# Kernel optimization log

Hardware: AMD Instinct MI355X
Metric: run time of the kernel (lower is better)

The kernel has to match this reference:

```python
import jax, jax.numpy as jnp
import numpy as np

B, S, E, H, DH, F = 4, 2048, 1024, 4, 256, 4096


def setup_inputs() -> dict:
    key = jax.random.key(0)
    ks = jax.random.split(key, 16)
    def w(k, shape):
        return jax.random.normal(k, shape, jnp.float32) * 0.02
    return {
        "inputs": jax.random.normal(ks[0], (B, S, E), jnp.float32),
        "context": jax.random.normal(ks[1], (B, S, E), jnp.float32),
        # self-attention (causal) per-head projections stacked over heads
        "Wk1": w(ks[2], (H, E, DH)), "bk1": jnp.zeros((H, DH), jnp.float32),
        "Wq1": w(ks[3], (H, E, DH)), "bq1": jnp.zeros((H, DH), jnp.float32),
        "Wv1": w(ks[4], (H, E, DH)), "bv1": jnp.zeros((H, DH), jnp.float32),
        "Wo1": w(ks[5], (E, E)), "bo1": jnp.zeros((E,), jnp.float32),
        # cross-attention (no mask)
        "Wk2": w(ks[6], (H, E, DH)), "bk2": jnp.zeros((H, DH), jnp.float32),
        "Wq2": w(ks[7], (H, E, DH)), "bq2": jnp.zeros((H, DH), jnp.float32),
        "Wv2": w(ks[8], (H, E, DH)), "bv2": jnp.zeros((H, DH), jnp.float32),
        "Wo2": w(ks[9], (E, E)), "bo2": jnp.zeros((E,), jnp.float32),
        "ln_g": jnp.ones((E,), jnp.float32), "ln_b": jnp.zeros((E,), jnp.float32),
        # FFN
        "W1": w(ks[10], (E, F)), "b1": jnp.zeros((F,), jnp.float32),
        "W2": w(ks[11], (F, E)), "b2": jnp.zeros((E,), jnp.float32),
    }


def _mha(kin, vin, qin, Wk, bk, Wq, bq, Wv, bv, Wo, bo, causal):
    # per-head Dense projections, batched over heads: [B,S,E] x [H,E,DH] -> [B,H,S,DH]
    K = jnp.einsum('bse,hed->bhsd', kin, Wk) + bk[None, :, None, :]
    Q = jnp.einsum('bse,hed->bhsd', qin, Wq) + bq[None, :, None, :]
    V = jnp.einsum('bse,hed->bhsd', vin, Wv) + bv[None, :, None, :]
    # NOTE: original divides by head_dim (K.get_shape()[2]), NOT sqrt(head_dim)
    scores = jnp.einsum('bhqd,bhkd->bhqk', Q, K) / K.shape[-1]
    if causal:
        sq, sk = scores.shape[-2], scores.shape[-1]
        mask = jnp.triu(jnp.full((sq, sk), -jnp.inf, scores.dtype), k=1)
        scores = scores + mask  # additive -inf strictly above the diagonal
    A = jax.nn.softmax(scores, axis=-1)
    # concat heads in order along the feature axis, then output Dense
    out = jnp.einsum('bhqk,bhkd->bqhd', A, V).reshape(qin.shape[0], qin.shape[1], -1)
    return out @ Wo + bo


def _ln(x, g, b):
    # keras LayerNormalization default epsilon = 1e-3
    m = x.mean(-1, keepdims=True)
    v = ((x - m) ** 2).mean(-1, keepdims=True)
    return (x - m) / jnp.sqrt(v + 1e-3) * g + b


def reference(inputs, context, Wk1, bk1, Wq1, bq1, Wv1, bv1, Wo1, bo1,
              Wk2, bk2, Wq2, bq2, Wv2, bv2, Wo2, bo2,
              ln_g, ln_b, W1, b1, W2, b2):
    # dropout layers are identity at inference
    a = _mha(inputs, inputs, inputs, Wk1, bk1, Wq1, bq1, Wv1, bv1, Wo1, bo1, True) + inputs
    a = _ln(a, ln_g, ln_b)
    # cross-attention: keys/values = context, queries = normalized self-attn output
    c = _mha(context, context, a, Wk2, bk2, Wq2, bq2, Wv2, bv2, Wo2, bo2, False) + a
    c = _ln(c, ln_g, ln_b)
    h = jax.nn.relu(c @ W1 + b1) @ W2 + b2 + c
    return jax.nn.relu(_ln(h, ln_g, ln_b))
```

## Files before the change

kernel.cpp:

```cpp
#include <hip/hip_runtime.h>

#define DEV __device__ __forceinline__

typedef unsigned short u16;
typedef __bf16 bf16x8 __attribute__((ext_vector_type(8)));
typedef bf16x8 __attribute__((may_alias)) bf16x8a;
typedef float f32x4 __attribute__((ext_vector_type(4)));
typedef float f32x16 __attribute__((ext_vector_type(16)));

constexpr int NB = 4, NS = 2048, NE = 1024, NH = 4, NDH = 256, NF = 4096;
constexpr int NR = NB * NS;

DEV u16 f2bf(float f) {
  unsigned u = __float_as_uint(f);
  u += 0x7fff + ((u >> 16) & 1);
  return (u16)(u >> 16);
}

DEV f32x4 mfma16(bf16x8 a, bf16x8 b, f32x4 c) {
  return __builtin_amdgcn_mfma_f32_16x16x32_bf16(a, b, c, 0, 0, 0);
}
DEV f32x16 mfma32(bf16x8 a, bf16x8 b, f32x16 c) {
  return __builtin_amdgcn_mfma_f32_32x32x16_bf16(a, b, c, 0, 0, 0);
}

DEV bf16x8 ldfrag(const u16* p) { return *(const bf16x8a*)p; }

DEV void gload_lds16(const void* g, void* l) {
  __builtin_amdgcn_global_load_lds(
      (const __attribute__((address_space(1))) void*)g,
      (__attribute__((address_space(3))) void*)l, 16, 0, 0);
}

DEV void blockbar() {
  asm volatile("" ::: "memory");
  __builtin_amdgcn_s_barrier();
  asm volatile("" ::: "memory");
}

DEV unsigned packbf(float a, float b) {
  union { __bf16 h[2]; unsigned u; } x;
  x.h[0] = (__bf16)a; x.h[1] = (__bf16)b;
  return x.u;
}

__global__ void cast_f32_bf16(const float* __restrict__ in, u16* __restrict__ out, int n4) {
  int i = blockIdx.x * 256 + threadIdx.x;
  if (i >= n4) return;
  float4 v = ((const float4*)in)[i];
  ushort4 o;
  o.x = f2bf(v.x); o.y = f2bf(v.y); o.z = f2bf(v.z); o.w = f2bf(v.w);
  ((ushort4*)out)[i] = o;
}

__global__ void transpose_cast(const float* __restrict__ in, u16* __restrict__ out, int R, int C) {
  __shared__ float t[32][33];
  size_t base = (size_t)blockIdx.z * R * C;
  int c0 = blockIdx.x * 32, r0 = blockIdx.y * 32;
  int x = threadIdx.x;
  for (int yy = threadIdx.y; yy < 32; yy += 8)
    t[yy][x] = in[base + (size_t)(r0 + yy) * C + c0 + x];
  __syncthreads();
  for (int yy = threadIdx.y; yy < 32; yy += 8)
    out[base + (size_t)(c0 + yy) * R + r0 + x] = f2bf(t[x][yy]);
}

__global__ void transpose_cast6(const float* s0, const float* s1, const float* s2,
                                const float* s3, const float* s4, const float* s5,
                                u16* d0, u16* d1, u16* d2, u16* d3, u16* d4, u16* d5) {
  __shared__ float t[32][33];
  int z = blockIdx.z;
  int widx = z >> 2, hz = z & 3;
  const float* in; u16* out;
  switch (widx) {
    case 0: in = s0; out = d0; break;
    case 1: in = s1; out = d1; break;
    case 2: in = s2; out = d2; break;
    case 3: in = s3; out = d3; break;
    case 4: in = s4; out = d4; break;
    default: in = s5; out = d5; break;
  }
  size_t base = (size_t)hz * NE * NDH;
  int c0 = blockIdx.x * 32, r0 = blockIdx.y * 32;
  int x = threadIdx.x;
  for (int yy = threadIdx.y; yy < 32; yy += 8)
    t[yy][x] = in[base + (size_t)(r0 + yy) * NDH + c0 + x];
  __syncthreads();
  for (int yy = threadIdx.y; yy < 32; yy += 8)
    out[base + (size_t)(c0 + yy) * NE + r0 + x] = f2bf(t[x][yy]);
}

__global__ void transpose_cast2(const float* s0, const float* s1,
                                u16* d0, u16* d1) {
  __shared__ float t[32][33];
  const float* in = blockIdx.z ? s1 : s0;
  u16* out = blockIdx.z ? d1 : d0;
  int c0 = blockIdx.x * 32, r0 = blockIdx.y * 32;
  int x = threadIdx.x;
  for (int yy = threadIdx.y; yy < 32; yy += 8)
    t[yy][x] = in[(size_t)(r0 + yy) * NE + c0 + x];
  __syncthreads();
  for (int yy = threadIdx.y; yy < 32; yy += 8)
    out[(size_t)(c0 + yy) * NE + r0 + x] = f2bf(t[x][yy]);
}

__global__ void pack_bias(const float* b0, const float* b1, const float* b2,
                          const float* b3, const float* b4,
                          float* BQKV1, float* BKV2) {
  int x = blockIdx.x;
  int seg = x >> 2;
  int i = (x & 3) * 256 + threadIdx.x;
  switch (seg) {
    case 0: BQKV1[i] = b0[i]; break;
    case 1: BQKV1[1024 + i] = b1[i]; break;
    case 2: BQKV1[2048 + i] = b2[i]; break;
    case 3: BKV2[i] = b3[i]; break;
    default: BKV2[1024 + i] = b4[i]; break;
  }
}

__global__ void transpose_v(const u16* __restrict__ V, int vstride, u16* __restrict__ Vt) {
  __shared__ u16 t[32][34];
  int bh = blockIdx.z, b = bh >> 2, h = bh & (NH - 1);
  int s0 = blockIdx.x * 32, d0 = blockIdx.y * 32;
  int x = threadIdx.x;
  for (int yy = threadIdx.y; yy < 32; yy += 8)
    t[yy][x] = V[(size_t)(b * NS + s0 + yy) * vstride + h * NDH + d0 + x];
  __syncthreads();
  for (int yy = threadIdx.y; yy < 32; yy += 8)
    Vt[((size_t)bh * NDH + d0 + yy) * NS + s0 + x] = t[x][yy];
}

template<int OUTF32, int RELU>
__global__ __launch_bounds__(256, 2)
void gemm2b(const u16* __restrict__ A, const u16* __restrict__ Bt,
            const float* __restrict__ bias, const float* __restrict__ res,
            float* __restrict__ outF, u16* __restrict__ outB,
            int M, int N, int K)
{
  __shared__ __align__(16) u16 smem[32768];

  int tid = threadIdx.x, w = tid >> 6, lane = tid & 63;
  int lr = lane & 15, lk = lane >> 4;

  int flat = blockIdx.y * gridDim.x + blockIdx.x;
  int cpx = (gridDim.x * gridDim.y) >> 3;
  int swz = (flat & 7) * cpx + (flat >> 3);
  int bx = swz % gridDim.x, by = swz / gridDim.x;
  int rowBlk = by * 128, colBlk = bx * 128;

  f32x4 acc[8][2];
#pragma unroll
  for (int f = 0; f < 8; f++)
#pragma unroll
    for (int n = 0; n < 2; n++) acc[f][n] = (f32x4){0.f, 0.f, 0.f, 0.f};

  int srow = lane >> 3;
  int scol = ((lane & 7) ^ srow) * 8;

  const u16* gA = A + (size_t)rowBlk * K;
  const u16* gB = Bt + (size_t)colBlk * K;

  auto stageA = [&](int t, int p) {
#pragma unroll
    for (int j = 0; j < 4; j++) {
      int rbase = (w * 4 + j) * 8;
      gload_lds16(gA + (size_t)(rbase + srow) * K + (size_t)t * 64 + scol,
                  &smem[(p * 128 + rbase) * 64]);
    }
  };
  auto stageB = [&](int t, int p) {
#pragma unroll
    for (int j = 0; j < 4; j++) {
      int rbase = (w * 4 + j) * 8;
      gload_lds16(gB + (size_t)(rbase + srow) * K + (size_t)t * 64 + scol,
                  &smem[16384 + (p * 128 + rbase) * 64]);
    }
  };

  stageB(0, 0);
  asm volatile("" ::: "memory");
  stageA(0, 0);
  asm volatile("s_waitcnt vmcnt(0)" ::: "memory");
  blockbar();

  int NT = K >> 6;
  for (int t = 0; t < NT; t++) {
    int p = t & 1;
    if (t + 1 < NT) {
      stageB(t + 1, p ^ 1);
      asm volatile("" ::: "memory");
      stageA(t + 1, p ^ 1);
      asm volatile("" ::: "memory");
    }
    const u16* Ar = &smem[p * 8192];
    const u16* Br = &smem[16384 + p * 8192];
    bf16x8 bf[2][2], af[8][2];
#pragma unroll
    for (int n = 0; n < 2; n++)
#pragma unroll
      for (int s = 0; s < 2; s++) {
        int rowB = w * 32 + n * 16 + lr;
        bf[n][s] = ldfrag(&Br[rowB * 64 + (((s * 4 + lk) ^ (lr & 7)) * 8)]);
      }
#pragma unroll
    for (int f = 0; f < 8; f++)
#pragma unroll
      for (int s = 0; s < 2; s++) {
        int rowA = f * 16 + lr;
        af[f][s] = ldfrag(&Ar[rowA * 64 + (((s * 4 + lk) ^ (lr & 7)) * 8)]);
      }
    __builtin_amdgcn_s_setprio(1);
#pragma unroll
    for (int f = 0; f < 8; f++)
#pragma unroll
      for (int n = 0; n < 2; n++)
#pragma unroll
        for (int s = 0; s < 2; s++)
          acc[f][n] = mfma16(af[f][s], bf[n][s], acc[f][n]);
    __builtin_amdgcn_s_setprio(0);
    asm volatile("s_waitcnt vmcnt(0)" ::: "memory");
    blockbar();
  }

  int ocol0 = colBlk + w * 32;
#pragma unroll
  for (int n = 0; n < 2; n++) {
    int c = ocol0 + n * 16 + lr;
    float bv = bias[c];
#pragma unroll
    for (int f = 0; f < 8; f++) {
      int r0 = rowBlk + f * 16 + lk * 4;
#pragma unroll
      for (int j = 0; j < 4; j++) {
        float v = acc[f][n][j] + bv;
        if (OUTF32) v += res[(size_t)(r0 + j) * N + c];
        if (RELU) v = fmaxf(v, 0.f);
        if (OUTF32) outF[(size_t)(r0 + j) * N + c] = v;
        else        outB[(size_t)(r0 + j) * N + c] = f2bf(v);
      }
    }
  }
}

template<int CAUSAL, int SPLIT>
__global__ __launch_bounds__(512, 2)
void attn8w(const u16* __restrict__ Qp, int qstride,
            const u16* __restrict__ Kp, int kstride,
            const u16* __restrict__ Vt, u16* __restrict__ O,
            float* __restrict__ Op, float* __restrict__ ml)
{
  __shared__ __align__(16) u16 smem[65536];

  int bidx = blockIdx.x;
  int bh, qt, kt0, kt1;
  if (SPLIT) {
    int qtIdx = bidx >> 5;
    qt = 15 - qtIdx;
    int sub = bidx & 31;
    int half = sub >> 4;
    bh = sub & 15;
    kt0 = half ? (qt + 1) : 0;
    kt1 = half ? (2 * qt + 2) : (qt + 1);
  } else {
    bh = bidx & 15;
    qt = CAUSAL ? (15 - (bidx >> 4)) : (bidx >> 4);
    kt0 = 0;
    kt1 = CAUSAL ? (2 * qt + 2) : (NS / 64);
  }
  int b = bh >> 2, h = bh & 3;
  int tid = threadIdx.x, w = tid >> 6, lane = tid & 63;
  int L = lane & 31, hi = lane >> 5;
  int g = w >> 1, ks = w & 1;

  int qbase = qt * 128 + g * 32;

  const u16* qrow = Qp + (size_t)(b * NS + qbase + L) * qstride + h * NDH;
  bf16x8 qf[16];
#pragma unroll
  for (int s = 0; s < 16; s++) qf[s] = ldfrag(qrow + s * 16 + hi * 8);

  f32x16 oacc[8];
#pragma unroll
  for (int db = 0; db < 8; db++) oacc[db] = (f32x16){};
  float m = -1e30f, l = 0.f;

  constexpr float SC = 1.0f / NDH;

  const u16* kbase = Kp + (size_t)(b * NS) * kstride + h * NDH;
  const u16* vbase = Vt + (size_t)bh * NDH * NS;

  auto stage = [&](int kt, int buf) {
#pragma unroll
    for (int ii = 0; ii < 4; ii++) {
      int gi = w * 4 + ii;
      int krow = 2 * gi + hi;
      int kcol = L ^ (krow & 31);
      gload_lds16(kbase + (size_t)(kt * 64 + krow) * kstride + kcol * 8,
                  &smem[buf * 16384 + gi * 512]);
      int vd = gi * 8 + (lane >> 3);
      int vg = (lane & 7) ^ (vd & 7);
      gload_lds16(vbase + (size_t)vd * NS + kt * 64 + vg * 8,
                  &smem[32768 + buf * 16384 + gi * 512]);
    }
  };

  stage(kt0, 0);
  asm volatile("" ::: "memory");

  for (int kt = kt0; kt < kt1; kt++) {
    int buf = (kt - kt0) & 1;
    const u16* bK = &smem[buf * 16384];
    const u16* bV = &smem[32768 + buf * 16384];
    if (kt + 1 < kt1) {
      stage(kt + 1, buf ^ 1);
      asm volatile("s_waitcnt vmcnt(8)" ::: "memory");
    } else {
      asm volatile("s_waitcnt vmcnt(0)" ::: "memory");
    }
    blockbar();

    int ksub0 = kt * 64 + ks * 32;
    bool skip = CAUSAL && (ksub0 > qbase + 31);
    if (!skip) {
      bool domask = CAUSAL && (ksub0 + 31 > qbase);
      __builtin_amdgcn_s_setprio(1);
      f32x16 sa = (f32x16){};
#pragma unroll
      for (int s = 0; s < 16; s++) {
        int row = ks * 32 + L;
        bf16x8 kf = ldfrag(&bK[row * 256 + (((2 * s + hi) ^ L) & 31) * 8]);
        sa = mfma32(kf, qf[s], sa);
      }
      __builtin_amdgcn_s_setprio(0);

      float p[16];
      float tmax = -1e30f;
#pragma unroll
      for (int r = 0; r < 16; r++) {
        float v = sa[r] * SC;
        if (domask) {
          int key = ksub0 + (r & 3) + 8 * (r >> 2) + 4 * hi;
          if (key > qbase + L) v = -1e30f;
        }
        p[r] = v;
        tmax = fmaxf(tmax, v);
      }
      tmax = fmaxf(tmax, __shfl_xor(tmax, 32));

      float mn = m;
      if (!__all(tmax - m <= 5.0f)) {
        mn = fmaxf(m, tmax);
        float rs = __expf(m - mn);
        m = mn;
        l *= rs;
#pragma unroll
        for (int db = 0; db < 8; db++)
#pragma unroll
          for (int r = 0; r < 16; r++) oacc[db][r] *= rs;
      }
      float psum = 0.f;
#pragma unroll
      for (int r = 0; r < 16; r++) {
        p[r] = __expf(p[r] - mn);
        psum += p[r];
      }
      psum += __shfl_xor(psum, 32);
      l += psum;

      unsigned pk01 = packbf(p[0], p[1]),  pk23 = packbf(p[2], p[3]);
      unsigned pk45 = packbf(p[4], p[5]),  pk67 = packbf(p[6], p[7]);
      unsigned pk89 = packbf(p[8], p[9]),  pkab = packbf(p[10], p[11]);
      unsigned pkcd = packbf(p[12], p[13]), pkef = packbf(p[14], p[15]);
      unsigned s45 = (unsigned)__shfl_xor((int)pk45, 32);
      unsigned s67 = (unsigned)__shfl_xor((int)pk67, 32);
      unsigned s01 = (unsigned)__shfl_xor((int)pk01, 32);
      unsigned s23 = (unsigned)__shfl_xor((int)pk23, 32);
      unsigned scd = (unsigned)__shfl_xor((int)pkcd, 32);
      unsigned sef = (unsigned)__shfl_xor((int)pkef, 32);
      unsigned s89 = (unsigned)__shfl_xor((int)pk89, 32);
      unsigned sab = (unsigned)__shfl_xor((int)pkab, 32);
      union { unsigned u[4]; bf16x8 v; } fb0, fb1;
      fb0.u[0] = hi ? s45 : pk01;
      fb0.u[1] = hi ? s67 : pk23;
      fb0.u[2] = hi ? pk45 : s01;
      fb0.u[3] = hi ? pk67 : s23;
      fb1.u[0] = hi ? scd : pk89;
      fb1.u[1] = hi ? sef : pkab;
      fb1.u[2] = hi ? pkcd : s89;
      fb1.u[3] = hi ? pkef : sab;
      bf16x8 pb0 = fb0.v, pb1 = fb1.v;

      __builtin_amdgcn_s_setprio(1);
#pragma unroll
      for (int db = 0; db < 8; db++) {
        int vd = db * 32 + L;
        bf16x8 vf0 = ldfrag(&bV[vd * 64 + (((ks * 4 + hi) ^ (vd & 7)) & 7) * 8]);
        bf16x8 vf1 = ldfrag(&bV[vd * 64 + (((ks * 4 + 2 + hi) ^ (vd & 7)) & 7) * 8]);
        oacc[db] = mfma32(vf0, pb0, oacc[db]);
        oacc[db] = mfma32(vf1, pb1, oacc[db]);
      }
      __builtin_amdgcn_s_setprio(0);
    }
    blockbar();
  }

  float* fsm = (float*)smem;
  blockbar();
  if (hi == 0) { fsm[w * 64 + L * 2] = m; fsm[w * 64 + L * 2 + 1] = l; }
  asm volatile("s_waitcnt lgkmcnt(0)" ::: "memory");
  blockbar();
  float mb = fsm[(w ^ 1) * 64 + L * 2];
  float lb = fsm[(w ^ 1) * 64 + L * 2 + 1];
  float M = fmaxf(m, mb);
  float eo = __expf(m - M);
  float lt = l * eo + lb * __expf(mb - M);
  asm volatile("s_waitcnt lgkmcnt(0)" ::: "memory");
  blockbar();
  float* reg = fsm + g * 8192;
  if (w & 1) {
#pragma unroll
    for (int db = 0; db < 8; db++)
#pragma unroll
      for (int r = 0; r < 16; r++) {
        int d = db * 32 + (r & 3) + 8 * (r >> 2) + 4 * hi;
        reg[d * 32 + L] = oacc[db][r] * eo;
      }
  }
  asm volatile("s_waitcnt lgkmcnt(0)" ::: "memory");
  blockbar();
  if (!(w & 1)) {
    if (SPLIT) {
      float* OpB = Op + (size_t)bidx * 32768 + (size_t)(g * 32 + L) * 256;
      if (hi == 0) {
        ml[((size_t)bidx * 128 + g * 32 + L) * 2]     = M;
        ml[((size_t)bidx * 128 + g * 32 + L) * 2 + 1] = lt;
      }
#pragma unroll
      for (int db = 0; db < 8; db++) {
#pragma unroll
        for (int rq = 0; rq < 4; rq++) {
          int d0 = db * 32 + rq * 8 + hi * 4;
          float4 v;
          v.x = oacc[db][rq * 4 + 0] * eo + reg[(d0 + 0) * 32 + L];
          v.y = oacc[db][rq * 4 + 1] * eo + reg[(d0 + 1) * 32 + L];
          v.z = oacc[db][rq * 4 + 2] * eo + reg[(d0 + 2) * 32 + L];
          v.w = oacc[db][rq * 4 + 3] * eo + reg[(d0 + 3) * 32 + L];
          *(float4*)(OpB + d0) = v;
        }
      }
    } else {
      float inv = 1.f / lt;
      size_t orow = (size_t)(b * NS + qbase + L) * NE + h * NDH;
#pragma unroll
      for (int db = 0; db < 8; db++) {
#pragma unroll
        for (int rq = 0; rq < 4; rq++) {
          int d0 = db * 32 + rq * 8 + hi * 4;
          float a0 = (oacc[db][rq * 4 + 0] * eo + reg[(d0 + 0) * 32 + L]) * inv;
          float a1 = (oacc[db][rq * 4 + 1] * eo + reg[(d0 + 1) * 32 + L]) * inv;
          float a2 = (oacc[db][rq * 4 + 2] * eo + reg[(d0 + 2) * 32 + L]) * inv;
          float a3 = (oacc[db][rq * 4 + 3] * eo + reg[(d0 + 3) * 32 + L]) * inv;
          uint2 wv;
          wv.x = packbf(a0, a1);
          wv.y = packbf(a2, a3);
          *(uint2*)&O[orow + d0] = wv;
        }
      }
    }
  }
}

__global__ __launch_bounds__(256)
void merge_attn(const float* __restrict__ Op, const float* __restrict__ ml,
                u16* __restrict__ O)
{
  int blk = blockIdx.x;
  int qt = blk >> 4, bh = blk & 15;
  int b = bh >> 2, h = bh & 3;
  int p0 = (15 - qt) * 32 + bh;
  int p1 = p0 + 16;
  int tid = threadIdx.x;
  int row = tid >> 1;
  int dbase = (tid & 1) * 128;

  float m0 = ml[((size_t)p0 * 128 + row) * 2];
  float l0 = ml[((size_t)p0 * 128 + row) * 2 + 1];
  float m1 = ml[((size_t)p1 * 128 + row) * 2];
  float l1 = ml[((size_t)p1 * 128 + row) * 2 + 1];
  float M = fmaxf(m0, m1);
  float e0 = __expf(m0 - M), e1 = __expf(m1 - M);
  float inv = 1.f / (l0 * e0 + l1 * e1);
  const float* O0 = Op + ((size_t)p0 * 128 + row) * 256 + dbase;
  const float* O1 = Op + ((size_t)p1 * 128 + row) * 256 + dbase;
  u16* dst = O + (size_t)(b * NS + qt * 128 + row) * NE + h * NDH + dbase;
#pragma unroll
  for (int d = 0; d < 128; d += 4) {
    float4 a = *(const float4*)(O0 + d);
    float4 c = *(const float4*)(O1 + d);
    uint2 wv;
    wv.x = packbf((a.x * e0 + c.x * e1) * inv, (a.y * e0 + c.y * e1) * inv);
    wv.y = packbf((a.z * e0 + c.z * e1) * inv, (a.w * e0 + c.w * e1) * inv);
    *(uint2*)(dst + d) = wv;
  }
}

template<int RELU, int WBF>
__global__ __launch_bounds__(256)
void ln_kernel(const float* __restrict__ x, const float* __restrict__ g,
               const float* __restrict__ bb, float* __restrict__ outF,
               u16* __restrict__ outB)
{
  int row = blockIdx.x, tid = threadIdx.x;
  float4 v = ((const float4*)(x + (size_t)row * NE))[tid];
  float s = v.x + v.y + v.z + v.w;
  float s2 = v.x * v.x + v.y * v.y + v.z * v.z + v.w * v.w;
#pragma unroll
  for (int off = 32; off; off >>= 1) {
    s += __shfl_xor(s, off);
    s2 += __shfl_xor(s2, off);
  }
  __shared__ float red[8];
  int wid = tid >> 6, lane = tid & 63;
  if (lane == 0) { red[wid] = s; red[4 + wid] = s2; }
  __syncthreads();
  s = red[0] + red[1] + red[2] + red[3];
  s2 = red[4] + red[5] + red[6] + red[7];
  float mean = s * (1.f / NE);
  float var = s2 * (1.f / NE) - mean * mean;
  float rstd = rsqrtf(var + 1e-3f);
  float4 gg = ((const float4*)g)[tid];
  float4 bv = ((const float4*)bb)[tid];
  float4 o;
  o.x = (v.x - mean) * rstd * gg.x + bv.x;
  o.y = (v.y - mean) * rstd * gg.y + bv.y;
  o.z = (v.z - mean) * rstd * gg.z + bv.z;
  o.w = (v.w - mean) * rstd * gg.w + bv.w;
  if (RELU) {
    o.x = fmaxf(o.x, 0.f); o.y = fmaxf(o.y, 0.f);
    o.z = fmaxf(o.z, 0.f); o.w = fmaxf(o.w, 0.f);
  }
  ((float4*)(outF + (size_t)row * NE))[tid] = o;
  if (WBF) {
    ushort4 ob;
    ob.x = f2bf(o.x); ob.y = f2bf(o.y); ob.z = f2bf(o.z); ob.w = f2bf(o.w);
    ((ushort4*)(outB + (size_t)row * NE))[tid] = ob;
  }
}

constexpr size_t OFF_X    = 0;
constexpr size_t OFF_W    = OFF_X + 16777216;
constexpr size_t OFF_BIAS = OFF_W + 33554432;
constexpr size_t OFF_QKV  = OFF_BIAS + 32768;
constexpr size_t OFF_VT   = OFF_QKV + 50331648;
constexpr size_t OFF_T0   = OFF_VT + 16777216;
constexpr size_t OFF_A    = OFF_T0 + 33554432;
constexpr size_t OFF_ABF  = OFF_A + 33554432;

extern "C" void kernel_launch(void* const* d_in, const int* in_sizes, int n_in,
                              void* d_out, int out_size, void* d_ws, size_t ws_size,
                              hipStream_t stream) {
  (void)in_sizes; (void)n_in; (void)out_size; (void)ws_size;
  const float* inp = (const float*)d_in[0];
  const float* ctx = (const float*)d_in[1];
  const float* Wk1 = (const float*)d_in[2];  const float* bk1 = (const float*)d_in[3];
  const float* Wq1 = (const float*)d_in[4];  const float* bq1 = (const float*)d_in[5];
  const float* Wv1 = (const float*)d_in[6];  const float* bv1 = (const float*)d_in[7];
  const float* Wo1 = (const float*)d_in[8];  const float* bo1 = (const float*)d_in[9];
  const float* Wk2 = (const float*)d_in[10]; const float* bk2 = (const float*)d_in[11];
  const float* Wq2 = (const float*)d_in[12]; const float* bq2 = (const float*)d_in[13];
  const float* Wv2 = (const float*)d_in[14]; const float* bv2 = (const float*)d_in[15];
  const float* Wo2 = (const float*)d_in[16]; const float* bo2 = (const float*)d_in[17];
  const float* lng = (const float*)d_in[18]; const float* lnb = (const float*)d_in[19];
  const float* W1  = (const float*)d_in[20]; const float* b1  = (const float*)d_in[21];
  const float* W2  = (const float*)d_in[22]; const float* b2  = (const float*)d_in[23];
  float* out = (float*)d_out;
  char* ws = (char*)d_ws;

  u16* XBF    = (u16*)(ws + OFF_X);
  u16* WQKV1T = (u16*)(ws + OFF_W);
  u16* WKV2T  = WQKV1T + 3072 * 1024;
  u16* WQ2T   = WKV2T + 2048 * 1024;
  u16* WO1T   = WQ2T + 1024 * 1024;
  u16* WO2T   = WO1T + 1024 * 1024;
  u16* W1T    = WO2T + 1024 * 1024;
  u16* W2T    = W1T + 4096 * 1024;
  float* BQKV1 = (float*)(ws + OFF_BIAS);
  float* BKV2  = BQKV1 + 3072;
  u16* QKV  = (u16*)(ws + OFF_QKV);
  u16* Q2   = QKV + 8192 * 2048;
  u16* VT   = (u16*)(ws + OFF_VT);
  u16* MID  = QKV;
  float* T0 = (float*)(ws + OFF_T0);
  float* OpBuf = T0;
  float* Af = (float*)(ws + OFF_A);
  u16* ABF  = (u16*)(ws + OFF_ABF);
  float* MlBuf = (float*)(ws + OFF_ABF);
  u16* Obuf = XBF;

  dim3 tb(32, 8);

  cast_f32_bf16<<<8192, 256, 0, stream>>>(inp, XBF, NR * NE / 4);
  transpose_cast6<<<dim3(8, 32, 24), tb, 0, stream>>>(
      Wk1, Wq1, Wv1, Wk2, Wv2, Wq2,
      WQKV1T, WQKV1T + 1024 * 1024, WQKV1T + 2048 * 1024,
      WKV2T, WKV2T + 1024 * 1024, WQ2T);
  transpose_cast2<<<dim3(32, 32, 2), tb, 0, stream>>>(Wo1, Wo2, WO1T, WO2T);
  transpose_cast<<<dim3(128, 32, 1), tb, 0, stream>>>(W1, W1T, NE, NF);
  transpose_cast<<<dim3(32, 128, 1), tb, 0, stream>>>(W2, W2T, NF, NE);
  pack_bias<<<20, 256, 0, stream>>>(bk1, bq1, bv1, bk2, bv2, BQKV1, BKV2);

  gemm2b<0, 0><<<dim3(24, 64), 256, 0, stream>>>(XBF, WQKV1T, BQKV1, nullptr,
                                                 nullptr, QKV, NR, 3072, NE);
  transpose_v<<<dim3(64, 8, 16), tb, 0, stream>>>(QKV + 2048, 3072, VT);
  attn8w<1, 1><<<512, 512, 0, stream>>>(QKV + 1024, 3072, QKV, 3072, VT,
                                        nullptr, OpBuf, MlBuf);
  merge_attn<<<256, 256, 0, stream>>>(OpBuf, MlBuf, Obuf);
  gemm2b<1, 0><<<dim3(8, 64), 256, 0, stream>>>(Obuf, WO1T, bo1, inp,
                                                T0, nullptr, NR, NE, NE);
  ln_kernel<0, 1><<<NR, 256, 0, stream>>>(T0, lng, lnb, Af, ABF);

  cast_f32_bf16<<<8192, 256, 0, stream>>>(ctx, XBF, NR * NE / 4);
  gemm2b<0, 0><<<dim3(16, 64), 256, 0, stream>>>(XBF, WKV2T, BKV2, nullptr,
                                                 nullptr, QKV, NR, 2048, NE);
  gemm2b<0, 0><<<dim3(8, 64), 256, 0, stream>>>(ABF, WQ2T, bq2, nullptr,
                                                nullptr, Q2, NR, NE, NE);
  transpose_v<<<dim3(64, 8, 16), tb, 0, stream>>>(QKV + 1024, 2048, VT);
  attn8w<0, 0><<<256, 512, 0, stream>>>(Q2, 1024, QKV, 2048, VT, Obuf,
                                        nullptr, nullptr);
  gemm2b<1, 0><<<dim3(8, 64), 256, 0, stream>>>(Obuf, WO2T, bo2, Af,
                                                T0, nullptr, NR, NE, NE);
  ln_kernel<0, 1><<<NR, 256, 0, stream>>>(T0, lng, lnb, Af, ABF);

  gemm2b<0, 1><<<dim3(32, 64), 256, 0, stream>>>(ABF, W1T, b1, nullptr,
                                                 nullptr, MID, NR, NF, NE);
  gemm2b<1, 0><<<dim3(8, 64), 256, 0, stream>>>(MID, W2T, b2, Af,
                                                T0, nullptr, NR, NE, NF);
  ln_kernel<1, 0><<<NR, 256, 0, stream>>>(T0, lng, lnb, out, nullptr);
}
```

Before: 697.9 us.

## Add single-buffered causal attention kernel with halved LDS for higher occupancy

Splits the causal split-K attention path into a dedicated kernel that single-buffers K and V tiles in half the shared memory (64KB instead of 128KB) and declares launch bounds for 4 blocks per CU. K for the next tile is prefetched while softmax runs, and V is reloaded after the PV product, with the epilogue reduction done in two halves to fit the smaller LDS. The cross-attention kernel loses its template parameters and becomes the non-causal specialization. The aim is to raise occupancy to hide latency, at the cost of extra barriers and less overlap between loads and compute, plus possible register pressure from the tighter launch bound.

```diff
diff --git a/kernel.cpp b/kernel.cpp
--- a/kernel.cpp
+++ b/kernel.cpp
@@ -243,31 +243,17 @@
   }
 }
 
-template<int CAUSAL, int SPLIT>
 __global__ __launch_bounds__(512, 2)
 void attn8w(const u16* __restrict__ Qp, int qstride,
             const u16* __restrict__ Kp, int kstride,
-            const u16* __restrict__ Vt, u16* __restrict__ O,
-            float* __restrict__ Op, float* __restrict__ ml)
+            const u16* __restrict__ Vt, u16* __restrict__ O)
 {
   __shared__ __align__(16) u16 smem[65536];
 
   int bidx = blockIdx.x;
-  int bh, qt, kt0, kt1;
-  if (SPLIT) {
-    int qtIdx = bidx >> 5;
-    qt = 15 - qtIdx;
-    int sub = bidx & 31;
-    int half = sub >> 4;
-    bh = sub & 15;
-    kt0 = half ? (qt + 1) : 0;
-    kt1 = half ? (2 * qt + 2) : (qt + 1);
-  } else {
-    bh = bidx & 15;
-    qt = CAUSAL ? (15 - (bidx >> 4)) : (bidx >> 4);
-    kt0 = 0;
-    kt1 = CAUSAL ? (2 * qt + 2) : (NS / 64);
-  }
+  int bh = bidx & 15;
+  int qt = bidx >> 4;
+  int kt0 = 0, kt1 = NS / 64;
   int b = bh >> 2, h = bh & 3;
   int tid = threadIdx.x, w = tid >> 6, lane = tid & 63;
   int L = lane & 31, hi = lane >> 5;
@@ -320,10 +306,7 @@
     }
     blockbar();
 
-    int ksub0 = kt * 64 + ks * 32;
-    bool skip = CAUSAL && (ksub0 > qbase + 31);
-    if (!skip) {
-      bool domask = CAUSAL && (ksub0 + 31 > qbase);
+    {
       __builtin_amdgcn_s_setprio(1);
       f32x16 sa = (f32x16){};
 #pragma unroll
@@ -339,10 +322,6 @@
 #pragma unroll
       for (int r = 0; r < 16; r++) {
         float v = sa[r] * SC;
-        if (domask) {
-          int key = ksub0 + (r & 3) + 8 * (r >> 2) + 4 * hi;
-          if (key > qbase + L) v = -1e30f;
-        }
         p[r] = v;
         tmax = fmaxf(tmax, v);
       }
@@ -430,41 +409,239 @@
   asm volatile("s_waitcnt lgkmcnt(0)" ::: "memory");
   blockbar();
   if (!(w & 1)) {
-    if (SPLIT) {
-      float* OpB = Op + (size_t)bidx * 32768 + (size_t)(g * 32 + L) * 256;
-      if (hi == 0) {
-        ml[((size_t)bidx * 128 + g * 32 + L) * 2]     = M;
-        ml[((size_t)bidx * 128 + g * 32 + L) * 2 + 1] = lt;
-      }
+    float inv = 1.f / lt;
+    size_t orow = (size_t)(b * NS + qbase + L) * NE + h * NDH;
+#pragma unroll
+    for (int db = 0; db < 8; db++) {
+#pragma unroll
+      for (int rq = 0; rq < 4; rq++) {
+        int d0 = db * 32 + rq * 8 + hi * 4;
+        float a0 = (oacc[db][rq * 4 + 0] * eo + reg[(d0 + 0) * 32 + L]) * inv;
+        float a1 = (oacc[db][rq * 4 + 1] * eo + reg[(d0 + 1) * 32 + L]) * inv;
+        float a2 = (oacc[db][rq * 4 + 2] * eo + reg[(d0 + 2) * 32 + L]) * inv;
+        float a3 = (oacc[db][rq * 4 + 3] * eo + reg[(d0 + 3) * 32 + L]) * inv;
+        uint2 wv;
+        wv.x = packbf(a0, a1);
+        wv.y = packbf(a2, a3);
+        *(uint2*)&O[orow + d0] = wv;
+      }
+    }
+  }
+}
+
+__global__ __launch_bounds__(512, 4)
+void attn8w_sb(const u16* __restrict__ Qp, int qstride,
+               const u16* __restrict__ Kp, int kstride,
+               const u16* __restrict__ Vt,
+               float* __restrict__ Op, float* __restrict__ ml)
+{
+  __shared__ __align__(16) u16 smem[32768];
+
+  int bidx = blockIdx.x;
+  int qtIdx = bidx >> 5;
+  int qt = 15 - qtIdx;
+  int sub = bidx & 31;
+  int half0 = sub >> 4;
+  int bh = sub & 15;
+  int kt0 = half0 ? (qt + 1) : 0;
+  int kt1 = half0 ? (2 * qt + 2) : (qt + 1);
+  int b = bh >> 2, h = bh & 3;
+  int tid = threadIdx.x, w = tid >> 6, lane = tid & 63;
+  int L = lane & 31, hi = lane >> 5;
+  int g = w >> 1, ks = w & 1;
+
+  int qbase = qt * 128 + g * 32;
+
+  const u16* qrow = Qp + (size_t)(b * NS + qbase + L) * qstride + h * NDH;
+  bf16x8 qf[16];
+#pragma unroll
+  for (int s = 0; s < 16; s++) qf[s] = ldfrag(qrow + s * 16 + hi * 8);
+
+  f32x16 oacc[8];
+#pragma unroll
+  for (int db = 0; db < 8; db++) oacc[db] = (f32x16){};
+  float m = -1e30f, l = 0.f;
+
+  constexpr float SC = 1.0f / NDH;
+
+  const u16* kbase = Kp + (size_t)(b * NS) * kstride + h * NDH;
+  const u16* vbase = Vt + (size_t)bh * NDH * NS;
+
+  auto stageK = [&](int kt) {
+#pragma unroll
+    for (int ii = 0; ii < 4; ii++) {
+      int gi = w * 4 + ii;
+      int krow = 2 * gi + hi;
+      int kcol = L ^ (krow & 31);
+      gload_lds16(kbase + (size_t)(kt * 64 + krow) * kstride + kcol * 8,
+                  &smem[gi * 512]);
+    }
+  };
+  auto stageV = [&](int kt) {
+#pragma unroll
+    for (int ii = 0; ii < 4; ii++) {
+      int gi = w * 4 + ii;
+      int vd = gi * 8 + (lane >> 3);
+      int vg = (lane & 7) ^ (vd & 7);
+      gload_lds16(vbase + (size_t)vd * NS + kt * 64 + vg * 8,
+                  &smem[16384 + gi * 512]);
+    }
+  };
+
+  stageK(kt0);
+  asm volatile("" ::: "memory");
+  stageV(kt0);
+  asm volatile("s_waitcnt vmcnt(0)" ::: "memory");
+  blockbar();
+
+  for (int kt = kt0; kt < kt1; kt++) {
+    bool last = (kt + 1 == kt1);
+    int ksub0 = kt * 64 + ks * 32;
+    bool skip = (ksub0 > qbase + 31);
+    bool domask = !skip && (ksub0 + 31 > qbase);
+
+    f32x16 sa = (f32x16){};
+    if (!skip) {
+      __builtin_amdgcn_s_setprio(1);
+#pragma unroll
+      for (int s = 0; s < 16; s++) {
+        int row = ks * 32 + L;
+        bf16x8 kf = ldfrag(&smem[row * 256 + (((2 * s + hi) ^ L) & 31) * 8]);
+        sa = mfma32(kf, qf[s], sa);
+      }
+      __builtin_amdgcn_s_setprio(0);
+    }
+    blockbar();
+    if (!last) stageK(kt + 1);
+
+    bf16x8 pb0, pb1;
+    if (!skip) {
+      float p[16];
+      float tmax = -1e30f;
+#pragma unroll
+      for (int r = 0; r < 16; r++) {
+        float v = sa[r] * SC;
+        if (domask) {
+          int key = ksub0 + (r & 3) + 8 * (r >> 2) + 4 * hi;
+          if (key > qbase + L) v = -1e30f;
+        }
+        p[r] = v;
+        tmax = fmaxf(tmax, v);
+      }
+      tmax = fmaxf(tmax, __shfl_xor(tmax, 32));
+
+      float mn = m;
+      if (!__all(tmax - m <= 5.0f)) {
+        mn = fmaxf(m, tmax);
+        float rs = __expf(m - mn);
+        m = mn;
+        l *= rs;
+#pragma unroll
+        for (int db = 0; db < 8; db++)
+#pragma unroll
+          for (int r = 0; r < 16; r++) oacc[db][r] *= rs;
+      }
+      float psum = 0.f;
+#pragma unroll
+      for (int r = 0; r < 16; r++) {
+        p[r] = __expf(p[r] - mn);
+        psum += p[r];
+      }
+      psum += __shfl_xor(psum, 32);
+      l += psum;
+
+      unsigned pk01 = packbf(p[0], p[1]),  pk23 = packbf(p[2], p[3]);
+      unsigned pk45 = packbf(p[4], p[5]),  pk67 = packbf(p[6], p[7]);
+      unsigned pk89 = packbf(p[8], p[9]),  pkab = packbf(p[10], p[11]);
+      unsigned pkcd = packbf(p[12], p[13]), pkef = packbf(p[14], p[15]);
+      unsigned s45 = (unsigned)__shfl_xor((int)pk45, 32);
+      unsigned s67 = (unsigned)__shfl_xor((int)pk67, 32);
+      unsigned s01 = (unsigned)__shfl_xor((int)pk01, 32);
+      unsigned s23 = (unsigned)__shfl_xor((int)pk23, 32);
+      unsigned scd = (unsigned)__shfl_xor((int)pkcd, 32);
+      unsigned sef = (unsigned)__shfl_xor((int)pkef, 32);
+      unsigned s89 = (unsigned)__shfl_xor((int)pk89, 32);
+      unsigned sab = (unsigned)__shfl_xor((int)pkab, 32);
+      union { unsigned u[4]; bf16x8 v; } fb0, fb1;
+      fb0.u[0] = hi ? s45 : pk01;
+      fb0.u[1] = hi ? s67 : pk23;
+      fb0.u[2] = hi ? pk45 : s01;
+      fb0.u[3] = hi ? pk67 : s23;
+      fb1.u[0] = hi ? scd : pk89;
+      fb1.u[1] = hi ? sef : pkab;
+      fb1.u[2] = hi ? pkcd : s89;
+      fb1.u[3] = hi ? pkef : sab;
+      pb0 = fb0.v; pb1 = fb1.v;
+    }
+
+    if (!last) asm volatile("s_waitcnt vmcnt(4)" ::: "memory");
+    else       asm volatile("s_waitcnt vmcnt(0)" ::: "memory");
+    blockbar();
+
+    if (!skip) {
+      __builtin_amdgcn_s_setprio(1);
 #pragma unroll
       for (int db = 0; db < 8; db++) {
+        int vd = db * 32 + L;
+        bf16x8 vf0 = ldfrag(&smem[16384 + vd * 64 + (((ks * 4 + hi) ^ (vd & 7)) & 7) * 8]);
+        bf16x8 vf1 = ldfrag(&smem[16384 + vd * 64 + (((ks * 4 + 2 + hi) ^ (vd & 7)) & 7) * 8]);
+        oacc[db] = mfma32(vf0, pb0, oacc[db]);
+        oacc[db] = mfma32(vf1, pb1, oacc[db]);
+      }
+      __builtin_amdgcn_s_setprio(0);
+    }
+    blockbar();
+    if (!last) {
+      stageV(kt + 1);
+      asm volatile("s_waitcnt vmcnt(4)" ::: "memory");
+      blockbar();
+    }
+  }
+
+  float* fsm = (float*)smem;
+  blockbar();
+  if (hi == 0) { fsm[w * 64 + L * 2] = m; fsm[w * 64 + L * 2 + 1] = l; }
+  asm volatile("s_waitcnt lgkmcnt(0)" ::: "memory");
+  blockbar();
+  float mb = fsm[(w ^ 1) * 64 + L * 2];
+  float lb = fsm[(w ^ 1) * 64 + L * 2 + 1];
+  float M = fmaxf(m, mb);
+  float eo = __expf(m - M);
+  float lt = l * eo + lb * __expf(mb - M);
+  if (hi == 0 && !(w & 1)) {
+    ml[((size_t)bidx * 128 + g * 32 + L) * 2]     = M;
+    ml[((size_t)bidx * 128 + g * 32 + L) * 2 + 1] = lt;
+  }
+  float* reg = fsm + g * 4096;
+#pragma unroll
+  for (int half = 0; half < 2; half++) {
+    asm volatile("s_waitcnt lgkmcnt(0)" ::: "memory");
+    blockbar();
+    if (w & 1) {
+#pragma unroll
+      for (int db = 0; db < 4; db++) {
+#pragma unroll
+        for (int r = 0; r < 16; r++) {
+          int d = db * 32 + (r & 3) + 8 * (r >> 2) + 4 * hi;
+          reg[d * 32 + L] = oacc[half * 4 + db][r] * eo;
+        }
+      }
+    }
+    asm volatile("s_waitcnt lgkmcnt(0)" ::: "memory");
+    blockbar();
+    if (!(w & 1)) {
+      float* OpB = Op + (size_t)bidx * 32768 + (size_t)(g * 32 + L) * 256 + half * 128;
+#pragma unroll
+      for (int db = 0; db < 4; db++) {
 #pragma unroll
         for (int rq = 0; rq < 4; rq++) {
           int d0 = db * 32 + rq * 8 + hi * 4;
           float4 v;
-          v.x = oacc[db][rq * 4 + 0] * eo + reg[(d0 + 0) * 32 + L];
-          v.y = oacc[db][rq * 4 + 1] * eo + reg[(d0 + 1) * 32 + L];
-          v.z = oacc[db][rq * 4 + 2] * eo + reg[(d0 + 2) * 32 + L];
-          v.w = oacc[db][rq * 4 + 3] * eo + reg[(d0 + 3) * 32 + L];
+          v.x = oacc[half * 4 + db][rq * 4 + 0] * eo + reg[(d0 + 0) * 32 + L];
+          v.y = oacc[half * 4 + db][rq * 4 + 1] * eo + reg[(d0 + 1) * 32 + L];
+          v.z = oacc[half * 4 + db][rq * 4 + 2] * eo + reg[(d0 + 2) * 32 + L];
+          v.w = oacc[half * 4 + db][rq * 4 + 3] * eo + reg[(d0 + 3) * 32 + L];
           *(float4*)(OpB + d0) = v;
-        }
-      }
-    } else {
-      float inv = 1.f / lt;
-      size_t orow = (size_t)(b * NS + qbase + L) * NE + h * NDH;
-#pragma unroll
-      for (int db = 0; db < 8; db++) {
-#pragma unroll
-        for (int rq = 0; rq < 4; rq++) {
-          int d0 = db * 32 + rq * 8 + hi * 4;
-          float a0 = (oacc[db][rq * 4 + 0] * eo + reg[(d0 + 0) * 32 + L]) * inv;
-          float a1 = (oacc[db][rq * 4 + 1] * eo + reg[(d0 + 1) * 32 + L]) * inv;
-          float a2 = (oacc[db][rq * 4 + 2] * eo + reg[(d0 + 2) * 32 + L]) * inv;
-          float a3 = (oacc[db][rq * 4 + 3] * eo + reg[(d0 + 3) * 32 + L]) * inv;
-          uint2 wv;
-          wv.x = packbf(a0, a1);
-          wv.y = packbf(a2, a3);
-          *(uint2*)&O[orow + d0] = wv;
         }
       }
     }
@@ -613,8 +790,8 @@
   gemm2b<0, 0><<<dim3(24, 64), 256, 0, stream>>>(XBF, WQKV1T, BQKV1, nullptr,
                                                  nullptr, QKV, NR, 3072, NE);
   transpose_v<<<dim3(64, 8, 16), tb, 0, stream>>>(QKV + 2048, 3072, VT);
-  attn8w<1, 1><<<512, 512, 0, stream>>>(QKV + 1024, 3072, QKV, 3072, VT,
-                                        nullptr, OpBuf, MlBuf);
+  attn8w_sb<<<512, 512, 0, stream>>>(QKV + 1024, 3072, QKV, 3072, VT,
+                                     OpBuf, MlBuf);
   merge_attn<<<256, 256, 0, stream>>>(OpBuf, MlBuf, Obuf);
   gemm2b<1, 0><<<dim3(8, 64), 256, 0, stream>>>(Obuf, WO1T, bo1, inp,
                                                 T0, nullptr, NR, NE, NE);
@@ -626,8 +803,7 @@
   gemm2b<0, 0><<<dim3(8, 64), 256, 0, stream>>>(ABF, WQ2T, bq2, nullptr,
                                                 nullptr, Q2, NR, NE, NE);
   transpose_v<<<dim3(64, 8, 16), tb, 0, stream>>>(QKV + 1024, 2048, VT);
-  attn8w<0, 0><<<256, 512, 0, stream>>>(Q2, 1024, QKV, 2048, VT, Obuf,
-                                        nullptr, nullptr);
+  attn8w<<<256, 512, 0, stream>>>(Q2, 1024, QKV, 2048, VT, Obuf);
   gemm2b<1, 0><<<dim3(8, 64), 256, 0, stream>>>(Obuf, WO2T, bo2, Af,
                                                 T0, nullptr, NR, NE, NE);
   ln_kernel<0, 1><<<NR, 256, 0, stream>>>(T0, lng, lnb, Af, ABF);
```

Result: slower. 1.024 ms (+46.8%).
